# Kernel optimization log

Hardware: AMD Instinct MI355X
Metric: run time of the kernel (lower is better)

## Reference

```python
import jax, jax.numpy as jnp
import numpy as np

N, E, B = 100000, 640000, 2000
NODE_TYPES, EDGE_TYPES = 16, 5
ND, ED, EMB, L = 256, 128, 256, 3  # node_dim, edge_dim, emb_dim, num encoder blocks


def setup_inputs() -> dict:
    key = jax.random.key(0)
    ks = jax.random.split(key, 20)
    s = 0.02
    inp = {
        "h_node": jax.random.normal(ks[0], (N, NODE_TYPES), jnp.float32),
        "pos_node": jax.random.normal(ks[1], (N, 3), jnp.float32),
        "h_edge": jax.random.normal(ks[2], (E, EDGE_TYPES), jnp.float32),
        "W_node": jax.random.normal(ks[3], (NODE_TYPES, ND), jnp.float32) * s,
        "W_edge": jax.random.normal(ks[4], (EDGE_TYPES, ED), jnp.float32) * s,
        # per-block encoder params (stacked over L blocks)
        "W_eu": jax.random.normal(ks[5], (L, ED + 2 * ND + 1, ED), jnp.float32) * s,
        "b_eu": jnp.zeros((L, ED), jnp.float32),
        "W_msg": jax.random.normal(ks[6], (L, ND + ED, ND), jnp.float32) * s,
        "b_msg": jnp.zeros((L, ND), jnp.float32),
        "W_nu": jax.random.normal(ks[7], (L, 2 * ND, ND), jnp.float32) * s,
        "b_nu": jnp.zeros((L, ND), jnp.float32),
        # final MLP: in=ND+ED, hidden=2*EMB, out=EMB (num_layer=2)
        "Wf1": jax.random.normal(ks[8], (ND + ED, 2 * EMB), jnp.float32) * s,
        "bf1": jnp.zeros((2 * EMB,), jnp.float32),
        "Wf2": jax.random.normal(ks[9], (2 * EMB, EMB), jnp.float32) * s,
        "bf2": jnp.zeros((EMB,), jnp.float32),
        "edge_index": jax.random.randint(ks[10], (2, E), 0, N, jnp.int64),
        "batch_node": jnp.sort(jax.random.randint(ks[11], (N,), 0, B, jnp.int64)),
        "batch_edge": jnp.sort(jax.random.randint(ks[12], (E,), 0, B, jnp.int64)),
    }
    return inp


def _segment_mean(x, ids, num_segments):
    tot = jax.ops.segment_sum(x, ids, num_segments=num_segments)
    cnt = jax.ops.segment_sum(jnp.ones((x.shape[0], 1), x.dtype), ids,
                              num_segments=num_segments)
    return tot / jnp.maximum(cnt, 1.0)


def reference(h_node, pos_node, h_edge, W_node, W_edge, W_eu, b_eu,
              W_msg, b_msg, W_nu, b_nu, Wf1, bf1, Wf2, bf2,
              edge_index, batch_node, batch_edge):
    src, dst = edge_index[0], edge_index[1]
    # embed node / edge type features
    hn = h_node @ W_node            # [N, ND]
    he = h_edge @ W_edge            # [E, ED]
    # NodeEdgeNet: L message-passing blocks with geometric edge feature
    dist = jnp.linalg.norm(pos_node[dst] - pos_node[src], axis=-1,
                           keepdims=True)  # [E, 1]
    for l in range(L):
        e_in = jnp.concatenate([he, hn[src], hn[dst], dist], axis=-1)
        he = jax.nn.relu(e_in @ W_eu[l] + b_eu[l])                 # edge update
        msg = jax.nn.relu(jnp.concatenate([hn[src], he], axis=-1)
                          @ W_msg[l] + b_msg[l])                    # [E, ND]
        agg = jax.ops.segment_sum(msg, dst, num_segments=N)         # [N, ND]
        hn = hn + jax.nn.relu(jnp.concatenate([hn, agg], axis=-1)
                              @ W_nu[l] + b_nu[l])                  # node update
    # per-graph mean pooling (replaces python loop over k with segment mean)
    mean_n = _segment_mean(hn, batch_node, B)   # [B, ND]
    mean_e = _segment_mean(he, batch_edge, B)   # [B, ED]
    h_sub = jnp.concatenate([mean_n, mean_e], axis=-1)  # [B, ND+ED]
    emb = jax.nn.relu(h_sub @ Wf1 + bf1) @ Wf2 + bf2     # [B, EMB]
    return emb, batch_node
```

## Files before the change

kernel.cpp:

```cpp
#include <hip/hip_runtime.h>
#include <hip/hip_bf16.h>
#include <math.h>

#define NN 100000
#define NE 640000
#define NB 2000

typedef __attribute__((ext_vector_type(4))) float v4f;
typedef long long ll64;
#define MFMA8(a, b, c) __builtin_amdgcn_mfma_f32_16x16x32_fp8_fp8(a, b, c, 0, 0, 0)

#define INV_S 0.000244140625f
#define ASCL 16.0f
#define AINV 0.0625f

#if __has_builtin(__builtin_amdgcn_cvt_pk_fp8_f32) && __has_builtin(__builtin_amdgcn_cvt_f32_fp8)
#define HW_FP8 1
#else
#define HW_FP8 0
#endif

__device__ __forceinline__ int IDX(const void* p, size_t i, int is64) {
    return is64 ? (int)((const long long*)p)[i] : ((const int*)p)[i];
}
__device__ __forceinline__ int clampi(int v, int n) {
    return ((unsigned)v < (unsigned)n) ? v : 0;
}

__global__ void k_detect(const int* bn32, int* flag) {
    if (threadIdx.x == 0 && blockIdx.x == 0) {
        int is64 = 1;
        for (int k = 50001; k < 50401; k += 2)
            if (bn32[k] != 0) { is64 = 0; break; }
        *flag = is64;
    }
}

__device__ __forceinline__ unsigned sw_enc_fp8(float x) {
    unsigned s = (__float_as_uint(x) >> 24) & 0x80u;
    float ax = fminf(fabsf(x), 448.f);
    if (ax < 0.015625f) {
        unsigned m = (unsigned)(ax * 512.f + 0.5f);
        return s | m;
    }
    unsigned b = __float_as_uint(ax) + 0x00080000u;
    unsigned e = (b >> 23) - 120u;
    unsigned m = (b >> 20) & 7u;
    unsigned v = (e << 3) | m;
    if (v > 0x7Eu) v = 0x7Eu;
    return s | v;
}
__device__ __forceinline__ float sw_dec_fp8(unsigned b) {
    unsigned s = (b & 0x80u) << 24;
    unsigned e = (b >> 3) & 15u;
    unsigned m = b & 7u;
    if (e) return __uint_as_float(s | ((e + 120u) << 23) | (m << 20));
    float f = (float)m * 0.001953125f;
    return (b & 0x80u) ? -f : f;
}
__device__ __forceinline__ unsigned enc1(float x) {
#if HW_FP8
    return (unsigned)__builtin_amdgcn_cvt_pk_fp8_f32(x, x, 0, false) & 255u;
#else
    return sw_enc_fp8(x);
#endif
}
__device__ __forceinline__ unsigned encpk(float a, float b) {
#if HW_FP8
    return (unsigned)__builtin_amdgcn_cvt_pk_fp8_f32(a, b, 0, false) & 0xFFFFu;
#else
    return sw_enc_fp8(a) | (sw_enc_fp8(b) << 8);
#endif
}
__device__ __forceinline__ float dec1(unsigned b) {
#if HW_FP8
    return __builtin_amdgcn_cvt_f32_fp8((int)b, 0);
#else
    return sw_dec_fp8(b);
#endif
}
__device__ __forceinline__ float bf_f(unsigned short u) {
    return __uint_as_float((unsigned)u << 16);
}
__device__ __forceinline__ unsigned short f_to_bf(float x) {
    __hip_bfloat16 h = __float2bfloat16(x);
    return *(unsigned short*)&h;
}

__global__ __launch_bounds__(256) void k_node_embed(const float* __restrict__ h_node,
                                                    const float* __restrict__ W,
                                                    unsigned char* __restrict__ hn8) {
    __shared__ float sh[8][16];
    int t = threadIdx.x;
    int r0 = blockIdx.x * 8;
    if (t < 128) sh[t >> 4][t & 15] = h_node[r0 * 16 + t];
    float w[16];
#pragma unroll
    for (int k = 0; k < 16; ++k) w[k] = W[k * 256 + t];
    __syncthreads();
#pragma unroll
    for (int r = 0; r < 8; ++r) {
        float acc = 0.f;
#pragma unroll
        for (int k = 0; k < 16; ++k) acc += sh[r][k] * w[k];
        hn8[(size_t)(r0 + r) * 256 + t] = (unsigned char)enc1(ASCL * acc);
    }
}

__global__ __launch_bounds__(256) void k_edge_embed(const float* __restrict__ h_edge,
                                                    const float* __restrict__ W,
                                                    const int* __restrict__ perm,
                                                    unsigned char* __restrict__ he8) {
    __shared__ float sh[16][5];
    int t = threadIdx.x;
    int e0 = blockIdx.x * 16;
    if (t < 80) {
        int row = t / 5, col = t % 5;
        int e = perm[e0 + row];
        sh[row][col] = h_edge[(size_t)e * 5 + col];
    }
    int c = t & 127;
    int es = t >> 7;
    float w[5];
#pragma unroll
    for (int k = 0; k < 5; ++k) w[k] = W[k * 128 + c];
    __syncthreads();
#pragma unroll
    for (int e = 0; e < 8; ++e) {
        int ee = es * 8 + e;
        float acc = 0.f;
#pragma unroll
        for (int k = 0; k < 5; ++k) acc += sh[ee][k] * w[k];
        he8[(size_t)(e0 + ee) * 128 + c] = (unsigned char)enc1(ASCL * acc);
    }
}

__global__ __launch_bounds__(256) void k_tr_w1(const float* __restrict__ W,
                                               unsigned char* __restrict__ WT) {
    int i = blockIdx.x * 256 + threadIdx.x;
    if (i >= 3 * 128 * 128) return;
    int l = i / 16384, r = i % 16384;
    int n = r / 128, k = r % 128;
    WT[i] = (unsigned char)enc1(256.f * W[(size_t)l * 641 * 128 + (size_t)k * 128 + n]);
}
__global__ __launch_bounds__(256) void k_tr_w2(const float* __restrict__ W,
                                               unsigned char* __restrict__ WT) {
    int i = blockIdx.x * 256 + threadIdx.x;
    if (i >= 3 * 256 * 128) return;
    int l = i / 32768, r = i % 32768;
    int n = r / 128, k = r % 128;
    WT[i] = (unsigned char)enc1(256.f * W[(size_t)l * 384 * 256 + (size_t)(256 + k) * 256 + n]);
}
__global__ __launch_bounds__(256) void k_tr_nu(const float* __restrict__ W,
                                               unsigned char* __restrict__ WT) {
    int i = blockIdx.x * 256 + threadIdx.x;
    if (i >= 3 * 256 * 512) return;
    int l = i / 131072, r = i % 131072;
    int n = r / 512, k = r % 512;
    WT[i] = (unsigned char)enc1(256.f * W[(size_t)l * 512 * 256 + (size_t)k * 256 + n]);
}
__global__ __launch_bounds__(256) void k_tr_pre(const float* __restrict__ Weu,
                                                const float* __restrict__ Wmsg,
                                                unsigned char* __restrict__ WT) {
    int i = blockIdx.x * 256 + threadIdx.x;
    if (i >= 3 * 512 * 256) return;
    int l = i / 131072, r = i % 131072;
    int n = r / 256, k = r % 256;
    float w;
    if (n < 128)      w = Weu[(size_t)l * 641 * 128 + (size_t)(128 + k) * 128 + n];
    else if (n < 256) w = Weu[(size_t)l * 641 * 128 + (size_t)(384 + k) * 128 + (n - 128)];
    else              w = Wmsg[(size_t)l * 384 * 256 + (size_t)k * 256 + (n - 256)];
    WT[i] = (unsigned char)enc1(256.f * w);
}

__global__ __launch_bounds__(256) void k_hist(const void* __restrict__ ei,
                                              const int* __restrict__ flag,
                                              int* __restrict__ hist) {
    int e = blockIdx.x * 256 + threadIdx.x;
    if (e >= NE) return;
    int d = clampi(IDX(ei, (size_t)NE + e, *flag), NN);
    atomicAdd(&hist[d], 1);
}
__global__ __launch_bounds__(1024) void k_scan(const int* __restrict__ hist,
                                               int* __restrict__ rowptr) {
    __shared__ int part[1024];
    int t = threadIdx.x;
    const int C = 98;
    int s = 0;
    for (int j = 0; j < C; ++j) {
        int i = t * C + j;
        if (i < NN) s += hist[i];
    }
    part[t] = s;
    __syncthreads();
    if (t == 0) {
        int run = 0;
        for (int i = 0; i < 1024; ++i) { int v = part[i]; part[i] = run; run += v; }
    }
    __syncthreads();
    int run = part[t];
    for (int j = 0; j < C; ++j) {
        int i = t * C + j;
        if (i < NN) { rowptr[i] = run; run += hist[i]; }
    }
}
__global__ __launch_bounds__(256) void k_perm(const void* __restrict__ ei,
                                              const int* __restrict__ flag,
                                              const float* __restrict__ pos,
                                              int* __restrict__ cursor,
                                              int* __restrict__ perm,
                                              int* __restrict__ inv,
                                              int* __restrict__ srcs,
                                              int* __restrict__ dsts,
                                              float* __restrict__ dist_s) {
    int e = blockIdx.x * 256 + threadIdx.x;
    if (e >= NE) return;
    int is64 = *flag;
    int s = clampi(IDX(ei, (size_t)e, is64), NN);
    int d = clampi(IDX(ei, (size_t)NE + e, is64), NN);
    int p = atomicAdd(&cursor[d], 1);
    perm[p] = e;
    inv[e] = p;
    srcs[p] = s;
    dsts[p] = d;
    float dx = pos[d * 3 + 0] - pos[s * 3 + 0];
    float dy = pos[d * 3 + 1] - pos[s * 3 + 1];
    float dz = pos[d * 3 + 2] - pos[s * 3 + 2];
    dist_s[p] = sqrtf(dx * dx + dy * dy + dz * dz);
}

#define NP_AS 264
__global__ __launch_bounds__(256, 3) void k_node_pre(
    const unsigned char* __restrict__ hn8, const unsigned char* __restrict__ WpreT,
    unsigned char* __restrict__ R) {
    __shared__ unsigned char s_A[64 * NP_AS];
    int t = threadIdx.x;
    int rb = blockIdx.x * 64;
    {
        int row = t >> 2, sb = t & 3;
        int gr = rb + row; if (gr >= NN) gr = NN - 1;
        const uint4* sp = (const uint4*)(hn8 + (size_t)gr * 256 + sb * 64);
        uint4 a = sp[0], b = sp[1], c = sp[2], d = sp[3];
        uint4* dp = (uint4*)&s_A[row * NP_AS + sb * 64];
        dp[0] = a; dp[1] = b; dp[2] = c; dp[3] = d;
    }
    __syncthreads();
    int lane = t & 63, wv = t >> 6, quad = lane >> 4, l16 = lane & 15;
    v4f zero4 = {0.f, 0.f, 0.f, 0.f};
#pragma unroll
    for (int pass = 0; pass < 2; ++pass) {
        int nt0 = wv * 8 + pass * 4;
        v4f acc[4][4];
#pragma unroll
        for (int mt = 0; mt < 4; ++mt)
#pragma unroll
            for (int nl = 0; nl < 4; ++nl) acc[mt][nl] = zero4;
#pragma unroll 2
        for (int k = 0; k < 256; k += 32) {
            int ko = k + quad * 8;
            ll64 b[4];
#pragma unroll
            for (int nl = 0; nl < 4; ++nl)
                b[nl] = *(const ll64*)(WpreT + (size_t)((nt0 + nl) * 16 + l16) * 256 + ko);
#pragma unroll
            for (int mt = 0; mt < 4; ++mt) {
                ll64 a = *(const ll64*)&s_A[(mt * 16 + l16) * NP_AS + ko];
#pragma unroll
                for (int nl = 0; nl < 4; ++nl) acc[mt][nl] = MFMA8(a, b[nl], acc[mt][nl]);
            }
        }
#pragma unroll
        for (int nl = 0; nl < 4; ++nl) {
            int c = (nt0 + nl) * 16 + l16;
#pragma unroll
            for (int mt = 0; mt < 4; ++mt)
#pragma unroll
                for (int rr = 0; rr < 2; ++rr) {
                    int rw0 = mt * 16 + quad * 4 + rr * 2;
                    unsigned pk = encpk(acc[mt][nl][rr * 2] * 0.00390625f,
                                        acc[mt][nl][rr * 2 + 1] * 0.00390625f);
                    if (rb + rw0 < NN)
                        R[(size_t)(rb + rw0) * 512 + c] = (unsigned char)(pk & 255u);
                    if (rb + rw0 + 1 < NN)
                        R[(size_t)(rb + rw0 + 1) * 512 + c] = (unsigned char)(pk >> 8);
                }
        }
    }
}

#define EF_S 136
#define EF_QS 264
#define EF_MS 264
__global__ __launch_bounds__(256, 4) void k_edge_fused(
    unsigned char* __restrict__ he8, const unsigned char* __restrict__ R,
    const float* __restrict__ dist_s,
    const int* __restrict__ srcs, const int* __restrict__ dsts,
    const unsigned char* __restrict__ W1T, const float* __restrict__ W_eu,
    const float* __restrict__ b_eu,
    const unsigned char* __restrict__ W2T, const float* __restrict__ b_msg,
    unsigned short* __restrict__ agg) {
    __shared__ __align__(16) unsigned char s_A[32 * EF_S];
    __shared__ __align__(16) unsigned char s_Pd[32 * EF_S];
    __shared__ __align__(16) unsigned char s_Ph[32 * EF_S];
    __shared__ __align__(16) unsigned char s_Q[32 * EF_QS];
    __shared__ __align__(16) unsigned short s_msg[32 * EF_MS];
    __shared__ float s_dist[32];
    __shared__ int s_dsti[32];
    int t = threadIdx.x;
    int eb = blockIdx.x * 32;
    int row = t >> 3, sb = t & 7;
    int sid = srcs[eb + row];
    int did = dsts[eb + row];
    if (t < 32) {
        s_dsti[t] = dsts[eb + t];
        s_dist[t] = dist_s[eb + t];
    }
    *(uint4*)&s_A[row * EF_S + sb * 16] =
        *(const uint4*)(he8 + (size_t)(eb + row) * 128 + sb * 16);
    *(uint4*)&s_Ph[row * EF_S + sb * 16] =
        *(const uint4*)(R + (size_t)sid * 512 + sb * 16);
    *(uint4*)&s_Pd[row * EF_S + sb * 16] =
        *(const uint4*)(R + (size_t)did * 512 + 128 + sb * 16);
    {
        const uint4* qp = (const uint4*)(R + (size_t)sid * 512 + 256 + sb * 32);
        uint4 q0 = qp[0], q1 = qp[1];
        *(uint4*)&s_Q[row * EF_QS + sb * 32] = q0;
        *(uint4*)&s_Q[row * EF_QS + sb * 32 + 16] = q1;
    }
    int lane = t & 63, wv = t >> 6, quad = lane >> 4, l16 = lane & 15;
    int n0 = wv * 2;
    const unsigned char* B0 = W1T + (size_t)(n0 * 16 + l16) * 128 + quad * 8;
    ll64 Brg[4][2];
#pragma unroll
    for (int kk = 0; kk < 4; ++kk) {
        Brg[kk][0] = *(const ll64*)(B0 + kk * 32);
        Brg[kk][1] = *(const ll64*)(B0 + 2048 + kk * 32);
    }
    __syncthreads();

    v4f zero4 = {0.f, 0.f, 0.f, 0.f};
    v4f acc[2][2];
    acc[0][0] = zero4; acc[0][1] = zero4; acc[1][0] = zero4; acc[1][1] = zero4;
#pragma unroll
    for (int kk = 0; kk < 4; ++kk) {
        int ko = kk * 32 + quad * 8;
#pragma unroll
        for (int mt = 0; mt < 2; ++mt) {
            ll64 a = *(const ll64*)&s_A[(mt * 16 + l16) * EF_S + ko];
            acc[mt][0] = MFMA8(a, Brg[kk][0], acc[mt][0]);
            acc[mt][1] = MFMA8(a, Brg[kk][1], acc[mt][1]);
        }
    }
#pragma unroll
    for (int nl = 0; nl < 2; ++nl) {
        int c = (n0 + nl) * 16 + l16;
        float w640 = W_eu[640 * 128 + c];
        float bb = b_eu[c];
#pragma unroll
        for (int mt = 0; mt < 2; ++mt)
#pragma unroll
            for (int rr = 0; rr < 2; ++rr) {
                int rw0 = mt * 16 + quad * 4 + rr * 2;
                int rw1 = rw0 + 1;
                float S0 = (dec1(s_Ph[rw0 * EF_S + c]) +
                            dec1(s_Pd[rw0 * EF_S + c])) * AINV;
                float S1 = (dec1(s_Ph[rw1 * EF_S + c]) +
                            dec1(s_Pd[rw1 * EF_S + c])) * AINV;
                float v0 = fmaxf(acc[mt][nl][rr * 2] * INV_S + S0 +
                                 s_dist[rw0] * w640 + bb, 0.f);
                float v1 = fmaxf(acc[mt][nl][rr * 2 + 1] * INV_S + S1 +
                                 s_dist[rw1] * w640 + bb, 0.f);
                unsigned pk = encpk(ASCL * v0, ASCL * v1);
                unsigned char q0 = (unsigned char)(pk & 255u);
                unsigned char q1 = (unsigned char)(pk >> 8);
                s_Ph[rw0 * EF_S + c] = q0;
                s_Ph[rw1 * EF_S + c] = q1;
                he8[(size_t)(eb + rw0) * 128 + c] = q0;
                he8[(size_t)(eb + rw1) * 128 + c] = q1;
            }
    }
    __syncthreads();

    v4f mac[2][4];
#pragma unroll
    for (int nl = 0; nl < 4; ++nl) { mac[0][nl] = zero4; mac[1][nl] = zero4; }
    int q0n = wv * 4;
#pragma unroll
    for (int kk = 0; kk < 4; ++kk) {
        int ko = kk * 32 + quad * 8;
        ll64 b[4];
#pragma unroll
        for (int nl = 0; nl < 4; ++nl)
            b[nl] = *(const ll64*)(W2T + (size_t)((q0n + nl) * 16 + l16) * 128 + ko);
#pragma unroll
        for (int mt = 0; mt < 2; ++mt) {
            ll64 a = *(const ll64*)&s_Ph[(mt * 16 + l16) * EF_S + ko];
#pragma unroll
            for (int nl = 0; nl < 4; ++nl) mac[mt][nl] = MFMA8(a, b[nl], mac[mt][nl]);
        }
    }
#pragma unroll
    for (int nl = 0; nl < 4; ++nl) {
        int c = (q0n + nl) * 16 + l16;
        float bm = b_msg[c];
#pragma unroll
        for (int mt = 0; mt < 2; ++mt)
#pragma unroll
            for (int r = 0; r < 4; ++r) {
                int rw = mt * 16 + quad * 4 + r;
                float qv = dec1(s_Q[rw * EF_QS + c]) * AINV;
                float v = fmaxf(mac[mt][nl][r] * INV_S + qv + bm, 0.f);
                s_msg[rw * EF_MS + c] = f_to_bf(v);
            }
    }
    __syncthreads();
    {
        int cp = t & 127;
        int half = t >> 7;
        int r0 = half * 16, r1 = r0 + 16;
        float ax = 0.f, ay = 0.f;
        int cur = s_dsti[r0];
        for (int rw = r0; rw < r1; ++rw) {
            int d2 = s_dsti[rw];
            if (d2 != cur) {
                if (ax != 0.f || ay != 0.f) {
                    __hip_bfloat162 pv;
                    pv.x = __float2bfloat16(ax);
                    pv.y = __float2bfloat16(ay);
                    unsafeAtomicAdd((__hip_bfloat162*)&agg[(size_t)cur * 256 + cp * 2], pv);
                }
                ax = 0.f; ay = 0.f; cur = d2;
            }
            unsigned v = *(const unsigned*)&s_msg[rw * EF_MS + cp * 2];
            ax += bf_f((unsigned short)(v & 0xFFFFu));
            ay += bf_f((unsigned short)(v >> 16));
        }
        if (ax != 0.f || ay != 0.f) {
            __hip_bfloat162 pv;
            pv.x = __float2bfloat16(ax);
            pv.y = __float2bfloat16(ay);
            unsafeAtomicAdd((__hip_bfloat162*)&agg[(size_t)cur * 256 + cp * 2], pv);
        }
    }
}

#define NF_AS 520
#define NF_BS 264
__global__ __launch_bounds__(256, 3) void k_node_fused(
    unsigned char* __restrict__ hn8, const unsigned short* __restrict__ agg,
    const unsigned char* __restrict__ WnuT, const float* __restrict__ b,
    const unsigned char* __restrict__ WpreT, unsigned char* __restrict__ R,
    int do_pre) {
    __shared__ unsigned char s_A[64 * NF_AS];
    __shared__ unsigned char s_B[64 * NF_BS];
    int t = threadIdx.x;
    int rb = blockIdx.x * 64;
    {
        int row = t >> 2, sb = t & 3;
        int gr = rb + row; if (gr >= NN) gr = NN - 1;
        const uint4* sp = (const uint4*)(hn8 + (size_t)gr * 256 + sb * 64);
        uint4 a = sp[0], b2 = sp[1], c = sp[2], d = sp[3];
        uint4* dp = (uint4*)&s_A[row * NF_AS + sb * 64];
        dp[0] = a; dp[1] = b2; dp[2] = c; dp[3] = d;
        const unsigned short* ap = agg + (size_t)gr * 256 + sb * 64;
        unsigned char* dq = &s_A[row * NF_AS + 256 + sb * 64];
#pragma unroll
        for (int j = 0; j < 64; j += 2) {
            unsigned pk = encpk(ASCL * bf_f(ap[j]), ASCL * bf_f(ap[j + 1]));
            *(unsigned short*)&dq[j] = (unsigned short)pk;
        }
    }
    __syncthreads();
    int lane = t & 63, wv = t >> 6, quad = lane >> 4, l16 = lane & 15;
    v4f zero4 = {0.f, 0.f, 0.f, 0.f};
    {
        v4f acc[4][4];
#pragma unroll
        for (int mt = 0; mt < 4; ++mt)
#pragma unroll
            for (int nl = 0; nl < 4; ++nl) acc[mt][nl] = zero4;
        int q0 = wv * 4;
#pragma unroll 2
        for (int k = 0; k < 512; k += 32) {
            int ko = k + quad * 8;
            ll64 b2[4];
#pragma unroll
            for (int nl = 0; nl < 4; ++nl)
                b2[nl] = *(const ll64*)(WnuT + (size_t)((q0 + nl) * 16 + l16) * 512 + ko);
#pragma unroll
            for (int mt = 0; mt < 4; ++mt) {
                ll64 a = *(const ll64*)&s_A[(mt * 16 + l16) * NF_AS + ko];
#pragma unroll
                for (int nl = 0; nl < 4; ++nl) acc[mt][nl] = MFMA8(a, b2[nl], acc[mt][nl]);
            }
        }
#pragma unroll
        for (int nl = 0; nl < 4; ++nl) {
            int c = (q0 + nl) * 16 + l16;
            float bv = b[c];
#pragma unroll
            for (int mt = 0; mt < 4; ++mt)
#pragma unroll
                for (int rr = 0; rr < 2; ++rr) {
                    int rw0 = mt * 16 + quad * 4 + rr * 2;
                    float o0 = dec1(s_A[rw0 * NF_AS + c]) * AINV;
                    float o1 = dec1(s_A[(rw0 + 1) * NF_AS + c]) * AINV;
                    float v0 = o0 + fmaxf(acc[mt][nl][rr * 2] * INV_S + bv, 0.f);
                    float v1 = o1 + fmaxf(acc[mt][nl][rr * 2 + 1] * INV_S + bv, 0.f);
                    unsigned pk = encpk(ASCL * v0, ASCL * v1);
                    unsigned char q0b = (unsigned char)(pk & 255u);
                    unsigned char q1b = (unsigned char)(pk >> 8);
                    s_B[rw0 * NF_BS + c] = q0b;
                    s_B[(rw0 + 1) * NF_BS + c] = q1b;
                    if (rb + rw0 < NN)
                        hn8[(size_t)(rb + rw0) * 256 + c] = q0b;
                    if (rb + rw0 + 1 < NN)
                        hn8[(size_t)(rb + rw0 + 1) * 256 + c] = q1b;
                }
        }
    }
    if (!do_pre) return;
    __syncthreads();
#pragma unroll
    for (int pass = 0; pass < 2; ++pass) {
        int nt0 = wv * 8 + pass * 4;
        v4f acc[4][4];
#pragma unroll
        for (int mt = 0; mt < 4; ++mt)
#pragma unroll
            for (int nl = 0; nl < 4; ++nl) acc[mt][nl] = zero4;
#pragma unroll 2
        for (int k = 0; k < 256; k += 32) {
            int ko = k + quad * 8;
            ll64 b2[4];
#pragma unroll
            for (int nl = 0; nl < 4; ++nl)
                b2[nl] = *(const ll64*)(WpreT + (size_t)((nt0 + nl) * 16 + l16) * 256 + ko);
#pragma unroll
            for (int mt = 0; mt < 4; ++mt) {
                ll64 a = *(const ll64*)&s_B[(mt * 16 + l16) * NF_BS + ko];
#pragma unroll
                for (int nl = 0; nl < 4; ++nl) acc[mt][nl] = MFMA8(a, b2[nl], acc[mt][nl]);
            }
        }
#pragma unroll
        for (int nl = 0; nl < 4; ++nl) {
            int c = (nt0 + nl) * 16 + l16;
#pragma unroll
            for (int mt = 0; mt < 4; ++mt)
#pragma unroll
                for (int rr = 0; rr < 2; ++rr) {
                    int rw0 = mt * 16 + quad * 4 + rr * 2;
                    unsigned pk = encpk(acc[mt][nl][rr * 2] * 0.00390625f,
                                        acc[mt][nl][rr * 2 + 1] * 0.00390625f);
                    if (rb + rw0 < NN)
                        R[(size_t)(rb + rw0) * 512 + c] = (unsigned char)(pk & 255u);
                    if (rb + rw0 + 1 < NN)
                        R[(size_t)(rb + rw0 + 1) * 512 + c] = (unsigned char)(pk >> 8);
                }
        }
    }
}

__device__ __forceinline__ int lbound(const void* a, int n, int v, int is64) {
    int lo = 0, hi = n;
    while (lo < hi) {
        int mid = (lo + hi) >> 1;
        if (IDX(a, mid, is64) < v) lo = mid + 1; else hi = mid;
    }
    return lo;
}

__global__ __launch_bounds__(512) void k_pool_mlp(
    const unsigned char* __restrict__ hn8, const unsigned char* __restrict__ he8,
    const int* __restrict__ inv,
    const void* __restrict__ bn, const void* __restrict__ be,
    const int* __restrict__ flag,
    const float* __restrict__ Wf1, const float* __restrict__ bf1,
    const float* __restrict__ Wf2, const float* __restrict__ bf2,
    float* __restrict__ out) {
    __shared__ float s_nacc[8][256];
    __shared__ float s_eacc[16][128];
    __shared__ float s_sub[384];
    __shared__ float s_hid[512];
    int b = blockIdx.x;
    int t = threadIdx.x;
    int is64 = *flag;
    int lane = t & 63, wv = t >> 6;
    int nlo = lbound(bn, NN, b, is64), nhi = lbound(bn, NN, b + 1, is64);
    int elo = lbound(be, NE, b, is64), ehi = lbound(be, NE, b + 1, is64);
    {
        float a0 = 0.f, a1 = 0.f, a2 = 0.f, a3 = 0.f;
        for (int i = nlo + wv; i < nhi; i += 8) {
            unsigned u = *(const unsigned*)(hn8 + (size_t)i * 256 + lane * 4);
            a0 += dec1(u & 255u);
            a1 += dec1((u >> 8) & 255u);
            a2 += dec1((u >> 16) & 255u);
            a3 += dec1(u >> 24);
        }
        s_nacc[wv][lane * 4 + 0] = a0;
        s_nacc[wv][lane * 4 + 1] = a1;
        s_nacc[wv][lane * 4 + 2] = a2;
        s_nacc[wv][lane * 4 + 3] = a3;
    }
    {
        int g16 = wv * 2 + (lane >> 5);
        int sl = lane & 31;
        float a0 = 0.f, a1 = 0.f, a2 = 0.f, a3 = 0.f;
        for (int e = elo + g16; e < ehi; e += 16) {
            int row = inv[e];
            unsigned u = *(const unsigned*)(he8 + (size_t)row * 128 + sl * 4);
            a0 += dec1(u & 255u);
            a1 += dec1((u >> 8) & 255u);
            a2 += dec1((u >> 16) & 255u);
            a3 += dec1(u >> 24);
        }
        s_eacc[g16][sl * 4 + 0] = a0;
        s_eacc[g16][sl * 4 + 1] = a1;
        s_eacc[g16][sl * 4 + 2] = a2;
        s_eacc[g16][sl * 4 + 3] = a3;
    }
    __syncthreads();
    if (t < 256) {
        float s = 0.f;
#pragma unroll
        for (int w = 0; w < 8; ++w) s += s_nacc[w][t];
        s_sub[t] = s * AINV / fmaxf((float)(nhi - nlo), 1.f);
    } else if (t < 384) {
        int c = t - 256;
        float s = 0.f;
#pragma unroll
        for (int j = 0; j < 16; ++j) s += s_eacc[j][c];
        s_sub[t] = s * AINV / fmaxf((float)(ehi - elo), 1.f);
    }
    __syncthreads();
    float hacc = bf1[t];
    for (int k = 0; k < 384; ++k) hacc += s_sub[k] * Wf1[k * 512 + t];
    s_hid[t] = fmaxf(hacc, 0.f);
    __syncthreads();
    if (t < 256) {
        float o = bf2[t];
        for (int k = 0; k < 512; ++k) o += s_hid[k] * Wf2[k * 256 + t];
        out[(size_t)b * 256 + t] = o;
    }
}

__global__ __launch_bounds__(256) void k_write_batch(const void* __restrict__ bn,
                                                     const int* __restrict__ flag,
                                                     float* __restrict__ out) {
    int i = blockIdx.x * 256 + threadIdx.x;
    if (i < NN) out[(size_t)NB * 256 + i] = (float)IDX(bn, i, *flag);
}

__global__ __launch_bounds__(256) void k_fill(float* __restrict__ p, int n, float v) {
    int i = blockIdx.x * 256 + threadIdx.x;
    if (i < n) p[i] = v;
}

extern "C" void kernel_launch(void* const* d_in, const int* in_sizes, int n_in,
                              void* d_out, int out_size, void* d_ws, size_t ws_size,
                              hipStream_t stream) {
    const float* h_node = (const float*)d_in[0];
    const float* pos    = (const float*)d_in[1];
    const float* h_edge = (const float*)d_in[2];
    const float* W_node = (const float*)d_in[3];
    const float* W_edge = (const float*)d_in[4];
    const float* W_eu   = (const float*)d_in[5];
    const float* b_eu   = (const float*)d_in[6];
    const float* W_msg  = (const float*)d_in[7];
    const float* b_msg  = (const float*)d_in[8];
    const float* W_nu   = (const float*)d_in[9];
    const float* b_nu   = (const float*)d_in[10];
    const float* Wf1    = (const float*)d_in[11];
    const float* bf1    = (const float*)d_in[12];
    const float* Wf2    = (const float*)d_in[13];
    const float* bf2    = (const float*)d_in[14];
    const void* ei = d_in[15];
    const void* bn = d_in[16];
    const void* be = d_in[17];

    float* out = (float*)d_out;

    const size_t SZ_FLAG = 256;
    const size_t SZ_HN   = (size_t)NN * 256;
    const size_t SZ_HE   = (size_t)NE * 128;
    const size_t SZ_AGG  = (size_t)NN * 256 * 2;
    const size_t SZ_R    = (size_t)NN * 512;
    const size_t SZ_PERM = (size_t)NE * 4;
    const size_t SZ_INV  = (size_t)NE * 4;
    const size_t SZ_SRC  = (size_t)NE * 4;
    const size_t SZ_DST  = (size_t)NE * 4;
    const size_t SZ_DS   = (size_t)NE * 4;
    const size_t SZ_PTR  = 512 * 1024;
    const size_t SZ_CUR  = 512 * 1024;
    const size_t SZ_W1   = (size_t)3 * 128 * 128;
    const size_t SZ_W2   = (size_t)3 * 256 * 128;
    const size_t SZ_WNU  = (size_t)3 * 256 * 512;
    const size_t SZ_WPRE = (size_t)3 * 512 * 256;
    const size_t NEED = SZ_FLAG + SZ_HN + SZ_HE + SZ_AGG + SZ_R + SZ_PERM +
                        SZ_INV + SZ_SRC + SZ_DST + SZ_DS + SZ_PTR + SZ_CUR +
                        SZ_W1 + SZ_W2 + SZ_WNU + SZ_WPRE;

    char* ws = (char*)d_ws;
    int* flag = (int*)ws;                       ws += SZ_FLAG;
    unsigned char* hn8 = (unsigned char*)ws;    ws += SZ_HN;
    unsigned char* he8 = (unsigned char*)ws;    ws += SZ_HE;
    unsigned short* agg = (unsigned short*)ws;  ws += SZ_AGG;
    unsigned char* R = (unsigned char*)ws;      ws += SZ_R;
    int* perm = (int*)ws;                       ws += SZ_PERM;
    int* inv = (int*)ws;                        ws += SZ_INV;
    int* srcs = (int*)ws;                       ws += SZ_SRC;
    int* dsts = (int*)ws;                       ws += SZ_DST;
    float* dist_s = (float*)ws;                 ws += SZ_DS;
    int* rowptr = (int*)ws;                     ws += SZ_PTR;
    int* cursor = (int*)ws;                     ws += SZ_CUR;
    unsigned char* W1T = (unsigned char*)ws;    ws += SZ_W1;
    unsigned char* W2T = (unsigned char*)ws;    ws += SZ_W2;
    unsigned char* WnuT = (unsigned char*)ws;   ws += SZ_WNU;
    unsigned char* WpreT = (unsigned char*)ws;  ws += SZ_WPRE;

    if (ws_size < NEED) {
        float enc = -(100000.0f + (float)(ws_size >> 20));
        k_detect<<<1, 64, 0, stream>>>((const int*)bn, flag);
        k_fill<<<(NB * 256 + 255) / 256, 256, 0, stream>>>(out, NB * 256, enc);
        k_write_batch<<<(NN + 255) / 256, 256, 0, stream>>>(bn, flag, out);
        return;
    }

    k_detect<<<1, 64, 0, stream>>>((const int*)bn, flag);
    k_tr_w1<<<(3 * 128 * 128 + 255) / 256, 256, 0, stream>>>(W_eu, W1T);
    k_tr_w2<<<(3 * 256 * 128 + 255) / 256, 256, 0, stream>>>(W_msg, W2T);
    k_tr_nu<<<(3 * 256 * 512 + 255) / 256, 256, 0, stream>>>(W_nu, WnuT);
    k_tr_pre<<<(3 * 512 * 256 + 255) / 256, 256, 0, stream>>>(W_eu, W_msg, WpreT);
    k_node_embed<<<NN / 8, 256, 0, stream>>>(h_node, W_node, hn8);

    hipMemsetAsync(cursor, 0, (size_t)NN * 4, stream);
    k_hist<<<(NE + 255) / 256, 256, 0, stream>>>(ei, flag, cursor);
    k_scan<<<1, 1024, 0, stream>>>(cursor, rowptr);
    hipMemcpyAsync(cursor, rowptr, (size_t)NN * 4, hipMemcpyDeviceToDevice, stream);
    k_perm<<<(NE + 255) / 256, 256, 0, stream>>>(ei, flag, pos, cursor, perm,
                                                 inv, srcs, dsts, dist_s);
    k_edge_embed<<<NE / 16, 256, 0, stream>>>(h_edge, W_edge, perm, he8);

    k_node_pre<<<(NN + 63) / 64, 256, 0, stream>>>(hn8, WpreT, R);

    for (int l = 0; l < 3; ++l) {
        hipMemsetAsync(agg, 0, SZ_AGG, stream);
        k_edge_fused<<<NE / 32, 256, 0, stream>>>(
            he8, R, dist_s, srcs, dsts,
            W1T + (size_t)l * 128 * 128, W_eu + (size_t)l * 641 * 128,
            b_eu + (size_t)l * 128,
            W2T + (size_t)l * 256 * 128, b_msg + (size_t)l * 256, agg);
        int do_pre = (l < 2) ? 1 : 0;
        const unsigned char* wpre_next = WpreT + (size_t)(do_pre ? (l + 1) : 0) * 512 * 256;
        k_node_fused<<<(NN + 63) / 64, 256, 0, stream>>>(
            hn8, agg, WnuT + (size_t)l * 256 * 512, b_nu + (size_t)l * 256,
            wpre_next, R, do_pre);
    }

    k_pool_mlp<<<NB, 512, 0, stream>>>(hn8, he8, inv, bn, be, flag,
                                       Wf1, bf1, Wf2, bf2, out);
    k_write_batch<<<(NN + 255) / 256, 256, 0, stream>>>(bn, flag, out);
}
```

Before: 1.776 ms.

## Stage fp8 outputs in LDS for coalesced stores; shrink edge messages to fp8

Edge and node kernels used to write he8, hn8 and R one byte at a time from MFMA fragments. They now stage those results in shared memory and write them with 16-byte vector stores after a barrier. In the edge kernel, messages are also stored in LDS as scaled fp8 instead of bf16. This halves the message buffer and allows a higher occupancy hint (6 waves). The cost is extra barriers and LDS traffic, some shared buffers being reused as scratch, and lower message precision before aggregation.

```diff
diff --git a/kernel.cpp b/kernel.cpp
--- a/kernel.cpp
+++ b/kernel.cpp
@@ -81,10 +81,6 @@
 }
 __device__ __forceinline__ float bf_f(unsigned short u) {
     return __uint_as_float((unsigned)u << 16);
-}
-__device__ __forceinline__ unsigned short f_to_bf(float x) {
-    __hip_bfloat16 h = __float2bfloat16(x);
-    return *(unsigned short*)&h;
 }
 
 __global__ __launch_bounds__(256) void k_node_embed(const float* __restrict__ h_node,
@@ -290,8 +286,8 @@
 
 #define EF_S 136
 #define EF_QS 264
-#define EF_MS 264
-__global__ __launch_bounds__(256, 4) void k_edge_fused(
+#define EF_MS 136
+__global__ __launch_bounds__(256, 6) void k_edge_fused(
     unsigned char* __restrict__ he8, const unsigned char* __restrict__ R,
     const float* __restrict__ dist_s,
     const int* __restrict__ srcs, const int* __restrict__ dsts,
@@ -303,7 +299,7 @@
     __shared__ __align__(16) unsigned char s_Pd[32 * EF_S];
     __shared__ __align__(16) unsigned char s_Ph[32 * EF_S];
     __shared__ __align__(16) unsigned char s_Q[32 * EF_QS];
-    __shared__ __align__(16) unsigned short s_msg[32 * EF_MS];
+    __shared__ __align__(16) unsigned char s_msg[32 * EF_MS];
     __shared__ float s_dist[32];
     __shared__ int s_dsti[32];
     int t = threadIdx.x;
@@ -371,15 +367,13 @@
                 float v1 = fmaxf(acc[mt][nl][rr * 2 + 1] * INV_S + S1 +
                                  s_dist[rw1] * w640 + bb, 0.f);
                 unsigned pk = encpk(ASCL * v0, ASCL * v1);
-                unsigned char q0 = (unsigned char)(pk & 255u);
-                unsigned char q1 = (unsigned char)(pk >> 8);
-                s_Ph[rw0 * EF_S + c] = q0;
-                s_Ph[rw1 * EF_S + c] = q1;
-                he8[(size_t)(eb + rw0) * 128 + c] = q0;
-                he8[(size_t)(eb + rw1) * 128 + c] = q1;
+                s_Ph[rw0 * EF_S + c] = (unsigned char)(pk & 255u);
+                s_Ph[rw1 * EF_S + c] = (unsigned char)(pk >> 8);
             }
     }
     __syncthreads();
+    *(uint4*)(he8 + (size_t)(eb + row) * 128 + sb * 16) =
+        *(const uint4*)&s_Ph[row * EF_S + sb * 16];
 
     v4f mac[2][4];
 #pragma unroll
@@ -406,11 +400,16 @@
 #pragma unroll
         for (int mt = 0; mt < 2; ++mt)
 #pragma unroll
-            for (int r = 0; r < 4; ++r) {
-                int rw = mt * 16 + quad * 4 + r;
-                float qv = dec1(s_Q[rw * EF_QS + c]) * AINV;
-                float v = fmaxf(mac[mt][nl][r] * INV_S + qv + bm, 0.f);
-                s_msg[rw * EF_MS + c] = f_to_bf(v);
+            for (int rr = 0; rr < 2; ++rr) {
+                int rw0 = mt * 16 + quad * 4 + rr * 2;
+                int rw1 = rw0 + 1;
+                float q0v = dec1(s_Q[rw0 * EF_QS + c]) * AINV;
+                float q1v = dec1(s_Q[rw1 * EF_QS + c]) * AINV;
+                float v0 = fmaxf(mac[mt][nl][rr * 2] * INV_S + q0v + bm, 0.f);
+                float v1 = fmaxf(mac[mt][nl][rr * 2 + 1] * INV_S + q1v + bm, 0.f);
+                unsigned pk = encpk(ASCL * v0, ASCL * v1);
+                s_msg[rw0 * EF_MS + c] = (unsigned char)(pk & 255u);
+                s_msg[rw1 * EF_MS + c] = (unsigned char)(pk >> 8);
             }
     }
     __syncthreads();
@@ -425,20 +424,20 @@
             if (d2 != cur) {
                 if (ax != 0.f || ay != 0.f) {
                     __hip_bfloat162 pv;
-                    pv.x = __float2bfloat16(ax);
-                    pv.y = __float2bfloat16(ay);
+                    pv.x = __float2bfloat16(ax * AINV);
+                    pv.y = __float2bfloat16(ay * AINV);
                     unsafeAtomicAdd((__hip_bfloat162*)&agg[(size_t)cur * 256 + cp * 2], pv);
                 }
                 ax = 0.f; ay = 0.f; cur = d2;
             }
-            unsigned v = *(const unsigned*)&s_msg[rw * EF_MS + cp * 2];
-            ax += bf_f((unsigned short)(v & 0xFFFFu));
-            ay += bf_f((unsigned short)(v >> 16));
+            unsigned short v = *(const unsigned short*)&s_msg[rw * EF_MS + cp * 2];
+            ax += dec1(v & 255u);
+            ay += dec1(v >> 8);
         }
         if (ax != 0.f || ay != 0.f) {
             __hip_bfloat162 pv;
-            pv.x = __float2bfloat16(ax);
-            pv.y = __float2bfloat16(ay);
+            pv.x = __float2bfloat16(ax * AINV);
+            pv.y = __float2bfloat16(ay * AINV);
             unsafeAtomicAdd((__hip_bfloat162*)&agg[(size_t)cur * 256 + cp * 2], pv);
         }
     }
@@ -455,15 +454,15 @@
     __shared__ unsigned char s_B[64 * NF_BS];
     int t = threadIdx.x;
     int rb = blockIdx.x * 64;
+    int row4 = t >> 2, sb4 = t & 3;
     {
-        int row = t >> 2, sb = t & 3;
-        int gr = rb + row; if (gr >= NN) gr = NN - 1;
-        const uint4* sp = (const uint4*)(hn8 + (size_t)gr * 256 + sb * 64);
+        int gr = rb + row4; if (gr >= NN) gr = NN - 1;
+        const uint4* sp = (const uint4*)(hn8 + (size_t)gr * 256 + sb4 * 64);
         uint4 a = sp[0], b2 = sp[1], c = sp[2], d = sp[3];
-        uint4* dp = (uint4*)&s_A[row * NF_AS + sb * 64];
+        uint4* dp = (uint4*)&s_A[row4 * NF_AS + sb4 * 64];
         dp[0] = a; dp[1] = b2; dp[2] = c; dp[3] = d;
-        const unsigned short* ap = agg + (size_t)gr * 256 + sb * 64;
-        unsigned char* dq = &s_A[row * NF_AS + 256 + sb * 64];
+        const unsigned short* ap = agg + (size_t)gr * 256 + sb4 * 64;
+        unsigned char* dq = &s_A[row4 * NF_AS + 256 + sb4 * 64];
 #pragma unroll
         for (int j = 0; j < 64; j += 2) {
             unsigned pk = encpk(ASCL * bf_f(ap[j]), ASCL * bf_f(ap[j + 1]));
@@ -508,19 +507,21 @@
                     float v0 = o0 + fmaxf(acc[mt][nl][rr * 2] * INV_S + bv, 0.f);
                     float v1 = o1 + fmaxf(acc[mt][nl][rr * 2 + 1] * INV_S + bv, 0.f);
                     unsigned pk = encpk(ASCL * v0, ASCL * v1);
-                    unsigned char q0b = (unsigned char)(pk & 255u);
-                    unsigned char q1b = (unsigned char)(pk >> 8);
-                    s_B[rw0 * NF_BS + c] = q0b;
-                    s_B[(rw0 + 1) * NF_BS + c] = q1b;
-                    if (rb + rw0 < NN)
-                        hn8[(size_t)(rb + rw0) * 256 + c] = q0b;
-                    if (rb + rw0 + 1 < NN)
-                        hn8[(size_t)(rb + rw0 + 1) * 256 + c] = q1b;
+                    s_B[rw0 * NF_BS + c] = (unsigned char)(pk & 255u);
+                    s_B[(rw0 + 1) * NF_BS + c] = (unsigned char)(pk >> 8);
                 }
         }
     }
+    __syncthreads();
+    if (rb + row4 < NN) {
+        const unsigned char* sp = &s_B[row4 * NF_BS + sb4 * 64];
+        uint4* dp = (uint4*)(hn8 + (size_t)(rb + row4) * 256 + sb4 * 64);
+        dp[0] = *(const uint4*)(sp);
+        dp[1] = *(const uint4*)(sp + 16);
+        dp[2] = *(const uint4*)(sp + 32);
+        dp[3] = *(const uint4*)(sp + 48);
+    }
     if (!do_pre) return;
-    __syncthreads();
 #pragma unroll
     for (int pass = 0; pass < 2; ++pass) {
         int nt0 = wv * 8 + pass * 4;
@@ -553,12 +554,17 @@
                     int rw0 = mt * 16 + quad * 4 + rr * 2;
                     unsigned pk = encpk(acc[mt][nl][rr * 2] * 0.00390625f,
                                         acc[mt][nl][rr * 2 + 1] * 0.00390625f);
-                    if (rb + rw0 < NN)
-                        R[(size_t)(rb + rw0) * 512 + c] = (unsigned char)(pk & 255u);
-                    if (rb + rw0 + 1 < NN)
-                        R[(size_t)(rb + rw0 + 1) * 512 + c] = (unsigned char)(pk >> 8);
+                    s_A[rw0 * NF_AS + c] = (unsigned char)(pk & 255u);
+                    s_A[(rw0 + 1) * NF_AS + c] = (unsigned char)(pk >> 8);
                 }
         }
+    }
+    __syncthreads();
+    if (rb + row4 < NN) {
+        const unsigned char* sp = &s_A[row4 * NF_AS + sb4 * 128];
+        uint4* dp = (uint4*)(R + (size_t)(rb + row4) * 512 + sb4 * 128);
+#pragma unroll
+        for (int j = 0; j < 8; ++j) dp[j] = *(const uint4*)(sp + j * 16);
     }
 }
 
```

Result: faster. 1.734 ms (-2.4%).
